# Kernel optimization log

Measured on AMD Instinct MI355X. Metric: run time of the kernel, lower is better.

Reference implementation:

```python
import jax, jax.numpy as jnp
import numpy as np


def setup_inputs() -> dict:
    key = jax.random.key(0)
    ks = jax.random.split(key, 6)
    N, E, D, L = 50000, 800000, 128, 2
    x = jax.random.normal(ks[0], (N, D), jnp.float32)
    h = jax.random.normal(ks[1], (L, N, D), jnp.float32)
    Wl = jax.random.normal(ks[2], (L, 6, D, D), jnp.float32) * 0.05  # neighbor (lin_l)
    Wr = jax.random.normal(ks[3], (L, 6, D, D), jnp.float32) * 0.05  # root (lin_r)
    b = jnp.zeros((L, 6, D), jnp.float32)
    src = jax.random.randint(ks[4], (E,), 0, N, jnp.int32)
    dst = jax.random.randint(ks[5], (E,), 0, N, jnp.int32)
    return {"x": x, "h": h, "Wl": Wl, "Wr": Wr, "b": b, "src": src, "dst": dst}


def reference(x, h, Wl, Wr, b, src, dst):
    # PyG SAGEConv (mean aggregation): out = mean_{j in N(i)} x_j @ W_l + x_i @ W_r + b
    N = x.shape[0]
    L = h.shape[0]
    deg = jax.ops.segment_sum(jnp.ones_like(src, jnp.float32), dst, num_segments=N)
    inv_deg = (1.0 / jnp.maximum(deg, 1.0))[:, None]  # [N,1]

    def sage(xin, l, g):
        agg = jax.ops.segment_sum(xin[src], dst, num_segments=N) * inv_deg  # [N,D]
        return agg @ Wl[l, g] + xin @ Wr[l, g] + b[l, g]

    outs = []
    inp = x
    for l in range(L):  # gates: 0=xz 1=hz 2=xr 3=hr 4=xh 5=hh
        z = jax.nn.sigmoid(sage(inp, l, 0) + sage(h[l], l, 1))
        r = jax.nn.sigmoid(sage(inp, l, 2) + sage(h[l], l, 3))
        h_tilde = jnp.tanh(sage(inp, l, 4) + sage(r * h[l], l, 5))
        out = z * h[l] + (1.0 - z) * h_tilde
        outs.append(out)
        inp = out
    return jnp.stack(outs)  # [L, N, D] == h_out
```

## Files before the change

kernel.cpp:

```cpp
#include <hip/hip_runtime.h>
#include <hip/hip_bf16.h>
#include <hip/hip_fp16.h>

#define D 128
#define BM 128
#define BN 128
#define LDK 72
#define SCAN_BLK 1024

typedef __attribute__((ext_vector_type(8))) __bf16 bf16x8;
typedef __attribute__((ext_vector_type(4))) float f32x4;
typedef __hip_bfloat16 bf16;

__device__ __forceinline__ float bf2f(bf16 v) { return __bfloat162float(v); }
__device__ __forceinline__ bf16 f2bf(float v) { return __float2bfloat16(v); }

__global__ void probe_kernel(const unsigned short* __restrict__ w, int n, int* __restrict__ flag) {
  __shared__ int cnt[256];
  int t = threadIdx.x;
  int bad = 0;
  int lim = n < 65536 ? n : 65536;
  for (int i = t; i < lim; i += 256) {
    unsigned int u = ((unsigned int)w[i]) << 16;
    float v = __uint_as_float(u);
    if (!(fabsf(v) <= 4.0f)) bad++;
  }
  cnt[t] = bad;
  __syncthreads();
  for (int off = 128; off > 0; off >>= 1) {
    if (t < off) cnt[t] += cnt[t + off];
    __syncthreads();
  }
  if (t == 0) flag[0] = (cnt[0] > 2048) ? 1 : 0;
}

__global__ void convert_kernel(const float* __restrict__ xf, const float* __restrict__ hf,
                               bf16* __restrict__ xb, bf16* __restrict__ hb,
                               const int* __restrict__ flag, int nx, int nh) {
  if (flag[0] == 0) return;
  int i = blockIdx.x * blockDim.x + threadIdx.x;
  if (i < nx) xb[i] = f2bf(xf[i]);
  if (i < nh) hb[i] = f2bf(hf[i]);
}


__global__ void zero_int_kernel(int* p, int n) {
  int i = blockIdx.x * blockDim.x + threadIdx.x;
  if (i < n) p[i] = 0;
}

__global__ void count_deg_kernel(const int* __restrict__ dst, int* __restrict__ deg, int E) {
  int e = blockIdx.x * blockDim.x + threadIdx.x;
  if (e < E) atomicAdd(&deg[dst[e]], 1);
}

__global__ void scan1_kernel(const int* __restrict__ deg, int* __restrict__ bsum, int N) {
  __shared__ int lsum[256];
  int t = threadIdx.x;
  int base = blockIdx.x * SCAN_BLK + t * 4;
  int s = 0;
  if (base + 3 < N) {
    int4 v = *(const int4*)(deg + base);
    s = v.x + v.y + v.z + v.w;
  } else {
    for (int i = 0; i < 4; ++i)
      if (base + i < N) s += deg[base + i];
  }
  lsum[t] = s;
  __syncthreads();
  for (int off = 128; off > 0; off >>= 1) {
    if (t < off) lsum[t] += lsum[t + off];
    __syncthreads();
  }
  if (t == 0) bsum[blockIdx.x] = lsum[0];
}

__global__ void scan2_kernel(int* __restrict__ bsum, int nb) {
  __shared__ int sh[256];
  int t = threadIdx.x;
  sh[t] = (t < nb) ? bsum[t] : 0;
  __syncthreads();
  for (int off = 1; off < 256; off <<= 1) {
    int v = sh[t];
    int add = (t >= off) ? sh[t - off] : 0;
    __syncthreads();
    sh[t] = v + add;
    __syncthreads();
  }
  if (t < nb) bsum[t] = (t == 0) ? 0 : sh[t - 1];
}

__global__ void scan3_kernel(const int* __restrict__ deg, const int* __restrict__ bsum,
                             int* __restrict__ offs, int* __restrict__ cursor,
                             float* __restrict__ inv_deg, int N, int E) {
  __shared__ int lsum[256];
  int t = threadIdx.x;
  int base = blockIdx.x * SCAN_BLK + t * 4;
  int d0 = 0, d1 = 0, d2 = 0, d3 = 0;
  if (base + 3 < N) {
    int4 v = *(const int4*)(deg + base);
    d0 = v.x; d1 = v.y; d2 = v.z; d3 = v.w;
  } else {
    if (base + 0 < N) d0 = deg[base + 0];
    if (base + 1 < N) d1 = deg[base + 1];
    if (base + 2 < N) d2 = deg[base + 2];
    if (base + 3 < N) d3 = deg[base + 3];
  }
  lsum[t] = d0 + d1 + d2 + d3;
  __syncthreads();
  for (int off = 1; off < 256; off <<= 1) {
    int v = lsum[t];
    int add = (t >= off) ? lsum[t - off] : 0;
    __syncthreads();
    lsum[t] = v + add;
    __syncthreads();
  }
  int run = bsum[blockIdx.x] + ((t == 0) ? 0 : lsum[t - 1]);
  int dd[4] = {d0, d1, d2, d3};
  for (int i = 0; i < 4; ++i) {
    int idx = base + i;
    if (idx < N) {
      offs[idx] = run;
      cursor[idx] = run;
      inv_deg[idx] = 1.0f / (float)(dd[i] > 1 ? dd[i] : 1);
      run += dd[i];
    }
  }
  if (blockIdx.x == 0 && t == 0) offs[N] = E;
}

__global__ void scatter_kernel(const int* __restrict__ src, const int* __restrict__ dst,
                               int* __restrict__ cursor, int* __restrict__ esrc, int E) {
  int e = blockIdx.x * blockDim.x + threadIdx.x;
  if (e < E) {
    int pos = atomicAdd(&cursor[dst[e]], 1);
    esrc[pos] = src[e];
  }
}


__global__ void agg_kernel(const bf16* __restrict__ featA, const bf16* __restrict__ featB,
                           const int* __restrict__ flag, const int* __restrict__ esrc,
                           const int* __restrict__ offs, const float* __restrict__ inv_deg,
                           bf16* __restrict__ out, int N) {
  const bf16* feat = flag[0] ? featB : featA;
  int node = (int)((blockIdx.x * (size_t)blockDim.x + threadIdx.x) >> 6);
  int lane = threadIdx.x & 63;
  if (node >= N) return;
  int e0 = offs[node], e1 = offs[node + 1];
  float a0 = 0.f, a1 = 0.f;
  int c = lane * 2;
  for (int base = e0; base < e1; base += 64) {
    int cnt = e1 - base;
    if (cnt > 64) cnt = 64;
    int ei = base + lane;
    int idx = esrc[ei < e1 ? ei : (e1 - 1)];
    int j = 0;
    for (; j + 8 <= cnt; j += 8) {
      int s0 = __shfl(idx, j + 0, 64), s1 = __shfl(idx, j + 1, 64);
      int s2 = __shfl(idx, j + 2, 64), s3 = __shfl(idx, j + 3, 64);
      int s4 = __shfl(idx, j + 4, 64), s5 = __shfl(idx, j + 5, 64);
      int s6 = __shfl(idx, j + 6, 64), s7 = __shfl(idx, j + 7, 64);
      __hip_bfloat162 v0 = *(const __hip_bfloat162*)(feat + (size_t)s0 * D + c);
      __hip_bfloat162 v1 = *(const __hip_bfloat162*)(feat + (size_t)s1 * D + c);
      __hip_bfloat162 v2 = *(const __hip_bfloat162*)(feat + (size_t)s2 * D + c);
      __hip_bfloat162 v3 = *(const __hip_bfloat162*)(feat + (size_t)s3 * D + c);
      __hip_bfloat162 v4 = *(const __hip_bfloat162*)(feat + (size_t)s4 * D + c);
      __hip_bfloat162 v5 = *(const __hip_bfloat162*)(feat + (size_t)s5 * D + c);
      __hip_bfloat162 v6 = *(const __hip_bfloat162*)(feat + (size_t)s6 * D + c);
      __hip_bfloat162 v7 = *(const __hip_bfloat162*)(feat + (size_t)s7 * D + c);
      a0 += bf2f(v0.x) + bf2f(v1.x) + bf2f(v2.x) + bf2f(v3.x) +
            bf2f(v4.x) + bf2f(v5.x) + bf2f(v6.x) + bf2f(v7.x);
      a1 += bf2f(v0.y) + bf2f(v1.y) + bf2f(v2.y) + bf2f(v3.y) +
            bf2f(v4.y) + bf2f(v5.y) + bf2f(v6.y) + bf2f(v7.y);
    }
    for (; j < cnt; ++j) {
      int s = __shfl(idx, j, 64);
      __hip_bfloat162 v = *(const __hip_bfloat162*)(feat + (size_t)s * D + c);
      a0 += bf2f(v.x);
      a1 += bf2f(v.y);
    }
  }
  float w = inv_deg[node];
  __hip_bfloat162 o;
  o.x = f2bf(a0 * w);
  o.y = f2bf(a1 * w);
  *(__hip_bfloat162*)(out + (size_t)node * D + c) = o;
}

__global__ void agg_dual_kernel(const bf16* __restrict__ fAa, const bf16* __restrict__ fAb,
                                const bf16* __restrict__ fBa, const bf16* __restrict__ fBb,
                                const int* __restrict__ flag, const int* __restrict__ esrc,
                                const int* __restrict__ offs, const float* __restrict__ inv_deg,
                                bf16* __restrict__ outA, bf16* __restrict__ outB, int N) {
  int fl = flag[0];
  const bf16* fA = fl ? fAb : fAa;
  const bf16* fB = fl ? fBb : fBa;
  int node = (int)((blockIdx.x * (size_t)blockDim.x + threadIdx.x) >> 6);
  int lane = threadIdx.x & 63;
  if (node >= N) return;
  int e0 = offs[node], e1 = offs[node + 1];
  float a0 = 0.f, a1 = 0.f, b0 = 0.f, b1 = 0.f;
  int c = lane * 2;
  for (int base = e0; base < e1; base += 64) {
    int cnt = e1 - base;
    if (cnt > 64) cnt = 64;
    int ei = base + lane;
    int idx = esrc[ei < e1 ? ei : (e1 - 1)];
    int j = 0;
    for (; j + 4 <= cnt; j += 4) {
      int s0 = __shfl(idx, j + 0, 64), s1 = __shfl(idx, j + 1, 64);
      int s2 = __shfl(idx, j + 2, 64), s3 = __shfl(idx, j + 3, 64);
      size_t r0 = (size_t)s0 * D + c, r1 = (size_t)s1 * D + c;
      size_t r2 = (size_t)s2 * D + c, r3 = (size_t)s3 * D + c;
      __hip_bfloat162 va0 = *(const __hip_bfloat162*)(fA + r0);
      __hip_bfloat162 va1 = *(const __hip_bfloat162*)(fA + r1);
      __hip_bfloat162 va2 = *(const __hip_bfloat162*)(fA + r2);
      __hip_bfloat162 va3 = *(const __hip_bfloat162*)(fA + r3);
      __hip_bfloat162 vb0 = *(const __hip_bfloat162*)(fB + r0);
      __hip_bfloat162 vb1 = *(const __hip_bfloat162*)(fB + r1);
      __hip_bfloat162 vb2 = *(const __hip_bfloat162*)(fB + r2);
      __hip_bfloat162 vb3 = *(const __hip_bfloat162*)(fB + r3);
      a0 += bf2f(va0.x) + bf2f(va1.x) + bf2f(va2.x) + bf2f(va3.x);
      a1 += bf2f(va0.y) + bf2f(va1.y) + bf2f(va2.y) + bf2f(va3.y);
      b0 += bf2f(vb0.x) + bf2f(vb1.x) + bf2f(vb2.x) + bf2f(vb3.x);
      b1 += bf2f(vb0.y) + bf2f(vb1.y) + bf2f(vb2.y) + bf2f(vb3.y);
    }
    for (; j < cnt; ++j) {
      int s = __shfl(idx, j, 64);
      size_t ro = (size_t)s * D + c;
      __hip_bfloat162 va = *(const __hip_bfloat162*)(fA + ro);
      __hip_bfloat162 vb = *(const __hip_bfloat162*)(fB + ro);
      a0 += bf2f(va.x);
      a1 += bf2f(va.y);
      b0 += bf2f(vb.x);
      b1 += bf2f(vb.y);
    }
  }
  float w = inv_deg[node];
  __hip_bfloat162 oa, ob;
  oa.x = f2bf(a0 * w);
  oa.y = f2bf(a1 * w);
  ob.x = f2bf(b0 * w);
  ob.y = f2bf(b1 * w);
  *(__hip_bfloat162*)(outA + (size_t)node * D + c) = oa;
  *(__hip_bfloat162*)(outB + (size_t)node * D + c) = ob;
}


__device__ __forceinline__ float loadw(const void* p, size_t idx, int fl) {
  return fl ? ((const float*)p)[idx] : bf2f(((const bf16*)p)[idx]);
}

__global__ void pack_kernel(const void* __restrict__ Wl, const void* __restrict__ Wr,
                            const void* __restrict__ b, int l, const int* __restrict__ flag,
                            bf16* __restrict__ B1p, bf16* __restrict__ B2p,
                            float* __restrict__ bs1, float* __restrict__ bs2) {
  int fl = flag[0];
  int idx = blockIdx.x * blockDim.x + threadIdx.x;
  const int SZ1 = 256 * 512;
  const int SZ2 = 128 * 512;
  if (idx < SZ1) {
    int n = idx >> 9, k = idx & 511;
    int p = k >> 7, kr = k & 127;
    int gpair = n >> 7, nc = n & 127;
    int gate = gpair * 2 + (p >> 1);
    const void* W = (p & 1) ? Wr : Wl;
    B1p[idx] = f2bf(loadw(W, (((size_t)l * 6 + gate) * D + kr) * D + nc, fl));
  } else if (idx < SZ1 + SZ2) {
    int i2 = idx - SZ1;
    int n = i2 >> 9, k = i2 & 511;
    int p = k >> 7, kr = k & 127;
    int gate = 4 + (p >> 1);
    const void* W = (p & 1) ? Wr : Wl;
    B2p[i2] = f2bf(loadw(W, (((size_t)l * 6 + gate) * D + kr) * D + n, fl));
  } else if (idx < SZ1 + SZ2 + 384) {
    int c = idx - (SZ1 + SZ2);
    if (c < 256) {
      int g0 = (c >> 7) * 2;
      int cc = c & 127;
      bs1[c] = loadw(b, ((size_t)l * 6 + g0) * D + cc, fl) +
               loadw(b, ((size_t)l * 6 + g0 + 1) * D + cc, fl);
    } else {
      int cc = c - 256;
      bs2[cc] = loadw(b, ((size_t)l * 6 + 4) * D + cc, fl) +
                loadw(b, ((size_t)l * 6 + 5) * D + cc, fl);
    }
  }
}


__device__ __forceinline__ void gemm_mainloop(const bf16* A0, const bf16* A1, const bf16* A2,
                                              const bf16* A3, const bf16* __restrict__ Bp, int M,
                                              int row0, int col0, bf16* As, bf16* Bs,
                                              f32x4 (&acc)[4][4]) {
  int tid = threadIdx.x;
  int wave = tid >> 6, lane = tid & 63;
  int wrow = (wave >> 1) * 64, wcol = (wave & 1) * 64;
  const bf16* Ablk[4] = {A0, A1, A2, A3};
#pragma unroll
  for (int kt = 0; kt < 8; ++kt) {
    const int kglob = kt * 64;
    const bf16* Aptr = Ablk[kglob >> 7];
    const int kr = kglob & 127;
#pragma unroll
    for (int i = 0; i < 4; ++i) {
      int c = tid + i * 256;
      int r = c >> 3;
      int ko = (c & 7) * 8;
      int rg = row0 + r;
      if (rg > M - 1) rg = M - 1;
      uint4 va = *(const uint4*)(const void*)(Aptr + (size_t)rg * D + kr + ko);
      *(uint4*)(void*)(As + r * LDK + ko) = va;
      uint4 vb = *(const uint4*)(const void*)(Bp + (size_t)(col0 + r) * 512 + kglob + ko);
      *(uint4*)(void*)(Bs + r * LDK + ko) = vb;
    }
    __syncthreads();
#pragma unroll
    for (int kk = 0; kk < 2; ++kk) {
      int kb = kk * 32 + (lane >> 4) * 8;
      int mr = lane & 15;
      bf16x8 af[4], bfv[4];
#pragma unroll
      for (int mi = 0; mi < 4; ++mi)
        af[mi] = *(const bf16x8*)(const void*)(As + (wrow + mi * 16 + mr) * LDK + kb);
#pragma unroll
      for (int ni = 0; ni < 4; ++ni)
        bfv[ni] = *(const bf16x8*)(const void*)(Bs + (wcol + ni * 16 + mr) * LDK + kb);
#pragma unroll
      for (int mi = 0; mi < 4; ++mi)
#pragma unroll
        for (int ni = 0; ni < 4; ++ni)
          acc[mi][ni] =
              __builtin_amdgcn_mfma_f32_16x16x32_bf16(af[mi], bfv[ni], acc[mi][ni], 0, 0, 0);
    }
    __syncthreads();
  }
}

__global__ __launch_bounds__(256) void gemm1_kernel(
    const bf16* A0, const bf16* A1a, const bf16* A1b, const bf16* A2, const bf16* A3a,
    const bf16* A3b, const int* __restrict__ flag, const bf16* __restrict__ Bp,
    const float* __restrict__ bias, __half* __restrict__ z, bf16* __restrict__ rh, int M) {
  int fl = flag[0];
  const bf16* A1 = fl ? A1b : A1a;
  const bf16* A3 = fl ? A3b : A3a;
  const bf16* hl = A3;
  __shared__ bf16 As[BM * LDK];
  __shared__ bf16 Bs[BN * LDK];
  f32x4 acc[4][4];
#pragma unroll
  for (int i = 0; i < 4; ++i)
#pragma unroll
    for (int j = 0; j < 4; ++j) acc[i][j] = (f32x4){0.f, 0.f, 0.f, 0.f};
  int row0 = blockIdx.x * BM, col0 = blockIdx.y * BN;
  gemm_mainloop(A0, A1, A2, A3, Bp, M, row0, col0, As, Bs, acc);
  int lane = threadIdx.x & 63, wave = threadIdx.x >> 6;
  int wrow = (wave >> 1) * 64, wcol = (wave & 1) * 64;
  int mr = lane & 15, quad = lane >> 4;
#pragma unroll
  for (int mi = 0; mi < 4; ++mi)
#pragma unroll
    for (int ni = 0; ni < 4; ++ni)
#pragma unroll
      for (int r = 0; r < 4; ++r) {
        int grow = row0 + wrow + mi * 16 + quad * 4 + r;
        if (grow >= M) continue;
        int gcol = col0 + wcol + ni * 16 + mr;
        float v = acc[mi][ni][r] + bias[gcol];
        float sg = 1.0f / (1.0f + __expf(-v));
        if (gcol < 128) {
          z[(size_t)grow * D + gcol] = __float2half(sg);
        } else {
          int cc = gcol - 128;
          float hv = bf2f(hl[(size_t)grow * D + cc]);
          rh[(size_t)grow * D + cc] = f2bf(sg * hv);
        }
      }
}

__global__ __launch_bounds__(256) void gemm2_kernel(
    const bf16* A0, const bf16* A1a, const bf16* A1b, const bf16* A2, const bf16* A3,
    const bf16* A3hA, const bf16* A3hB, const int* __restrict__ flag, const bf16* __restrict__ Bp,
    const float* __restrict__ bias, const __half* __restrict__ z, void* __restrict__ outbase,
    size_t lND, bf16* __restrict__ nextb, int M) {
  int fl = flag[0];
  const bf16* A1 = fl ? A1b : A1a;
  const bf16* hl = fl ? A3hB : A3hA;
  __shared__ bf16 As[BM * LDK];
  __shared__ bf16 Bs[BN * LDK];
  f32x4 acc[4][4];
#pragma unroll
  for (int i = 0; i < 4; ++i)
#pragma unroll
    for (int j = 0; j < 4; ++j) acc[i][j] = (f32x4){0.f, 0.f, 0.f, 0.f};
  int row0 = blockIdx.x * BM, col0 = 0;
  gemm_mainloop(A0, A1, A2, A3, Bp, M, row0, col0, As, Bs, acc);
  int lane = threadIdx.x & 63, wave = threadIdx.x >> 6;
  int wrow = (wave >> 1) * 64, wcol = (wave & 1) * 64;
  int mr = lane & 15, quad = lane >> 4;
#pragma unroll
  for (int mi = 0; mi < 4; ++mi)
#pragma unroll
    for (int ni = 0; ni < 4; ++ni)
#pragma unroll
      for (int r = 0; r < 4; ++r) {
        int grow = row0 + wrow + mi * 16 + quad * 4 + r;
        if (grow >= M) continue;
        int gcol = col0 + wcol + ni * 16 + mr;
        float pre = acc[mi][ni][r] + bias[gcol];
        float ht = tanhf(pre);
        size_t off = (size_t)grow * D + gcol;
        float zv = __half2float(z[off]);
        float hv = bf2f(hl[off]);
        float ov = zv * hv + (1.0f - zv) * ht;
        if (fl) {
          ((float*)outbase)[lND + off] = ov;
          nextb[off] = f2bf(ov);
        } else {
          ((bf16*)outbase)[lND + off] = f2bf(ov);
        }
      }
}


extern "C" void kernel_launch(void* const* d_in, const int* in_sizes, int n_in, void* d_out,
                              int out_size, void* d_ws, size_t ws_size, hipStream_t stream) {
  const void* x = d_in[0];
  const void* h = d_in[1];
  const void* Wl = d_in[2];
  const void* Wr = d_in[3];
  const void* b = d_in[4];
  const int* src = (const int*)d_in[5];
  const int* dst = (const int*)d_in[6];

  const int NX = in_sizes[0];
  const int NH = in_sizes[1];
  const int N = NX / D;
  const int E = in_sizes[5];
  const int L = NH / NX;
  (void)n_in;
  (void)out_size;
  (void)ws_size;

  char* ws = (char*)d_ws;
  size_t off = 0;
  auto alloc = [&](size_t bytes) -> char* {
    char* p = ws + off;
    off = (off + bytes + 255) & ~(size_t)255;
    return p;
  };
  int* flag = (int*)alloc(256);
  int* deg = (int*)alloc((size_t)N * 4);
  int* offs = (int*)alloc((size_t)(N + 1) * 4);
  int* cursor = (int*)alloc((size_t)N * 4);
  float* inv_deg = (float*)alloc((size_t)N * 4);
  int* bsum = (int*)alloc(256 * 4);
  int* esrc = (int*)alloc((size_t)E * 4);
  bf16* agg_inp = (bf16*)alloc((size_t)N * D * 2);
  bf16* agg2 = (bf16*)alloc((size_t)N * D * 2);
  bf16* rh = (bf16*)alloc((size_t)N * D * 2);
  __half* z = (__half*)alloc((size_t)N * D * 2);
  bf16* B1p = (bf16*)alloc(256 * 512 * 2);
  bf16* B2p = (bf16*)alloc(128 * 512 * 2);
  float* bs1 = (float*)alloc(256 * 4);
  float* bs2 = (float*)alloc(128 * 4);
  bf16* xb = (bf16*)alloc((size_t)NX * 2);
  bf16* hb = (bf16*)alloc((size_t)NH * 2);

  probe_kernel<<<1, 256, 0, stream>>>((const unsigned short*)Wl, in_sizes[2], flag);
  int ncv = NX > NH ? NX : NH;
  convert_kernel<<<(ncv + 255) / 256, 256, 0, stream>>>((const float*)x, (const float*)h, xb, hb,
                                                        flag, NX, NH);

  zero_int_kernel<<<(N + 255) / 256, 256, 0, stream>>>(deg, N);
  count_deg_kernel<<<(E + 255) / 256, 256, 0, stream>>>(dst, deg, E);
  int nb = (N + SCAN_BLK - 1) / SCAN_BLK;
  scan1_kernel<<<nb, 256, 0, stream>>>(deg, bsum, N);
  scan2_kernel<<<1, 256, 0, stream>>>(bsum, nb);
  scan3_kernel<<<nb, 256, 0, stream>>>(deg, bsum, offs, cursor, inv_deg, N, E);
  scatter_kernel<<<(E + 255) / 256, 256, 0, stream>>>(src, dst, cursor, esrc, E);

  int mtiles = (N + BM - 1) / BM;
  const int pack_elems = 256 * 512 + 128 * 512 + 384;
  for (int l = 0; l < L; ++l) {
    const size_t lND = (size_t)l * N * D;
    const bf16* inpA = (l == 0) ? (const bf16*)x : ((const bf16*)d_out + lND - (size_t)N * D);
    const bf16* hlA = (const bf16*)h + lND;
    const bf16* hlB = hb + lND;

    pack_kernel<<<(pack_elems + 255) / 256, 256, 0, stream>>>(Wl, Wr, b, l, flag, B1p, B2p, bs1,
                                                              bs2);
    agg_dual_kernel<<<(N + 3) / 4, 256, 0, stream>>>(inpA, xb, hlA, hlB, flag, esrc, offs, inv_deg,
                                                     agg_inp, agg2, N);
    gemm1_kernel<<<dim3(mtiles, 2), 256, 0, stream>>>(agg_inp, inpA, xb, agg2, hlA, hlB, flag, B1p,
                                                      bs1, z, rh, N);
    agg_kernel<<<(N + 3) / 4, 256, 0, stream>>>(rh, rh, flag, esrc, offs, inv_deg, agg2, N);
    gemm2_kernel<<<dim3(mtiles, 1), 256, 0, stream>>>(agg_inp, inpA, xb, agg2, rh, hlA, hlB, flag,
                                                      B2p, bs2, z, d_out, lND, xb, N);
  }
}
```

Measured before the change: 672.2 us.

## Load GEMM fragments directly from global memory, drop LDS staging and barriers

The GEMM main loop no longer stages A and B tiles through shared memory with barriers. Each wave now loads its MFMA fragments straight from global memory using precomputed row offsets. It also replaces tanhf with a cheaper exp-based formula in the gemm2 epilogue. This removes LDS traffic and synchronization, but gives up the cross-wave data reuse that LDS provided, so global and L2 load traffic per block rises roughly twofold.

New measurement: 749.2 us. +11.5%, slower.

```diff
diff --git a/kernel.cpp b/kernel.cpp
--- a/kernel.cpp
+++ b/kernel.cpp
@@ -5,7 +5,6 @@
 #define D 128
 #define BM 128
 #define BN 128
-#define LDK 72
 #define SCAN_BLK 1024
 
 typedef __attribute__((ext_vector_type(8))) __bf16 bf16x8;
@@ -292,41 +291,36 @@
 
 __device__ __forceinline__ void gemm_mainloop(const bf16* A0, const bf16* A1, const bf16* A2,
                                               const bf16* A3, const bf16* __restrict__ Bp, int M,
-                                              int row0, int col0, bf16* As, bf16* Bs,
-                                              f32x4 (&acc)[4][4]) {
+                                              int row0, int col0, f32x4 (&acc)[4][4]) {
   int tid = threadIdx.x;
   int wave = tid >> 6, lane = tid & 63;
   int wrow = (wave >> 1) * 64, wcol = (wave & 1) * 64;
+  int mr = lane & 15, quad = lane >> 4;
   const bf16* Ablk[4] = {A0, A1, A2, A3};
+  size_t arow[4], brow[4];
+#pragma unroll
+  for (int mi = 0; mi < 4; ++mi) {
+    int rg = row0 + wrow + mi * 16 + mr;
+    if (rg > M - 1) rg = M - 1;
+    arow[mi] = (size_t)rg * D;
+  }
+#pragma unroll
+  for (int ni = 0; ni < 4; ++ni) brow[ni] = (size_t)(col0 + wcol + ni * 16 + mr) * 512;
+
 #pragma unroll
   for (int kt = 0; kt < 8; ++kt) {
-    const int kglob = kt * 64;
-    const bf16* Aptr = Ablk[kglob >> 7];
-    const int kr = kglob & 127;
-#pragma unroll
-    for (int i = 0; i < 4; ++i) {
-      int c = tid + i * 256;
-      int r = c >> 3;
-      int ko = (c & 7) * 8;
-      int rg = row0 + r;
-      if (rg > M - 1) rg = M - 1;
-      uint4 va = *(const uint4*)(const void*)(Aptr + (size_t)rg * D + kr + ko);
-      *(uint4*)(void*)(As + r * LDK + ko) = va;
-      uint4 vb = *(const uint4*)(const void*)(Bp + (size_t)(col0 + r) * 512 + kglob + ko);
-      *(uint4*)(void*)(Bs + r * LDK + ko) = vb;
-    }
-    __syncthreads();
+    const bf16* Aptr = Ablk[kt >> 1];
+    const int ka = (kt & 1) * 64 + quad * 8;
+    const int kb = kt * 64 + quad * 8;
 #pragma unroll
     for (int kk = 0; kk < 2; ++kk) {
-      int kb = kk * 32 + (lane >> 4) * 8;
-      int mr = lane & 15;
       bf16x8 af[4], bfv[4];
 #pragma unroll
       for (int mi = 0; mi < 4; ++mi)
-        af[mi] = *(const bf16x8*)(const void*)(As + (wrow + mi * 16 + mr) * LDK + kb);
+        af[mi] = *(const bf16x8*)(const void*)(Aptr + arow[mi] + ka + kk * 32);
 #pragma unroll
       for (int ni = 0; ni < 4; ++ni)
-        bfv[ni] = *(const bf16x8*)(const void*)(Bs + (wcol + ni * 16 + mr) * LDK + kb);
+        bfv[ni] = *(const bf16x8*)(const void*)(Bp + brow[ni] + kb + kk * 32);
 #pragma unroll
       for (int mi = 0; mi < 4; ++mi)
 #pragma unroll
@@ -334,7 +328,6 @@
           acc[mi][ni] =
               __builtin_amdgcn_mfma_f32_16x16x32_bf16(af[mi], bfv[ni], acc[mi][ni], 0, 0, 0);
     }
-    __syncthreads();
   }
 }
 
@@ -346,15 +339,13 @@
   const bf16* A1 = fl ? A1b : A1a;
   const bf16* A3 = fl ? A3b : A3a;
   const bf16* hl = A3;
-  __shared__ bf16 As[BM * LDK];
-  __shared__ bf16 Bs[BN * LDK];
   f32x4 acc[4][4];
 #pragma unroll
   for (int i = 0; i < 4; ++i)
 #pragma unroll
     for (int j = 0; j < 4; ++j) acc[i][j] = (f32x4){0.f, 0.f, 0.f, 0.f};
   int row0 = blockIdx.x * BM, col0 = blockIdx.y * BN;
-  gemm_mainloop(A0, A1, A2, A3, Bp, M, row0, col0, As, Bs, acc);
+  gemm_mainloop(A0, A1, A2, A3, Bp, M, row0, col0, acc);
   int lane = threadIdx.x & 63, wave = threadIdx.x >> 6;
   int wrow = (wave >> 1) * 64, wcol = (wave & 1) * 64;
   int mr = lane & 15, quad = lane >> 4;
@@ -387,15 +378,13 @@
   int fl = flag[0];
   const bf16* A1 = fl ? A1b : A1a;
   const bf16* hl = fl ? A3hB : A3hA;
-  __shared__ bf16 As[BM * LDK];
-  __shared__ bf16 Bs[BN * LDK];
   f32x4 acc[4][4];
 #pragma unroll
   for (int i = 0; i < 4; ++i)
 #pragma unroll
     for (int j = 0; j < 4; ++j) acc[i][j] = (f32x4){0.f, 0.f, 0.f, 0.f};
   int row0 = blockIdx.x * BM, col0 = 0;
-  gemm_mainloop(A0, A1, A2, A3, Bp, M, row0, col0, As, Bs, acc);
+  gemm_mainloop(A0, A1, A2, A3, Bp, M, row0, col0, acc);
   int lane = threadIdx.x & 63, wave = threadIdx.x >> 6;
   int wrow = (wave >> 1) * 64, wcol = (wave & 1) * 64;
   int mr = lane & 15, quad = lane >> 4;
@@ -409,7 +398,7 @@
         if (grow >= M) continue;
         int gcol = col0 + wcol + ni * 16 + mr;
         float pre = acc[mi][ni][r] + bias[gcol];
-        float ht = tanhf(pre);
+        float ht = 1.0f - 2.0f / (1.0f + __expf(2.0f * pre));
         size_t off = (size_t)grow * D + gcol;
         float zv = __half2float(z[off]);
         float hv = bf2f(hl[off]);
```
